# Performance work log

Hardware: AMD Instinct MI355X
Metric: run time of the kernel (lower is better)

The kernel has to match this reference:

```python
import jax, jax.numpy as jnp
import numpy as np

DIM_Q = 1024
DIM_K = 1024
DIM_V = 1024


def setup_inputs() -> dict:
    key = jax.random.key(0)
    kx, kq, kk, kv = jax.random.split(key, 4)
    x = jax.random.normal(kx, (4, 2048, DIM_Q), dtype=jnp.float32)
    # torch nn.Linear weights: [out_features, in_features], y = x @ W.T
    scale = 1.0 / np.sqrt(DIM_Q)
    Wq = jax.random.uniform(kq, (DIM_K, DIM_Q), dtype=jnp.float32, minval=-scale, maxval=scale)
    Wk = jax.random.uniform(kk, (DIM_K, DIM_Q), dtype=jnp.float32, minval=-scale, maxval=scale)
    Wv = jax.random.uniform(kv, (DIM_V, DIM_Q), dtype=jnp.float32, minval=-scale, maxval=scale)
    return {"x": x, "Wq": Wq, "Wk": Wk, "Wv": Wv}


def reference(x, Wq, Wk, Wv):
    # q, k: [b, s, dim_k]; v: [b, s, dim_v]
    q = jnp.einsum('bsd,kd->bsk', x, Wq)
    k = jnp.einsum('bsd,kd->bsk', x, Wk)
    v = jnp.einsum('bsd,vd->bsv', x, Wv)
    norm_fact = 1.0 / jnp.sqrt(jnp.asarray(DIM_K, dtype=x.dtype))
    score = jnp.einsum('bik,bjk->bij', q, k) * norm_fact  # [b, s, s]
    score = jax.nn.softmax(score, axis=-1)
    att = jnp.einsum('bij,bjv->biv', score, v)
    att = att + v  # is_residual=True
    return att
```

## Files before the change

kernel.cpp:

```cpp
#include <hip/hip_runtime.h>
#include <hip/hip_bf16.h>

using bf16 = __hip_bfloat16;
typedef __attribute__((ext_vector_type(8))) short short8;
typedef __attribute__((ext_vector_type(4))) float floatx4;
typedef __attribute__((ext_vector_type(8))) int int8v;

__device__ __forceinline__ void async_ld16(const void* g, void* l) {
  __builtin_amdgcn_global_load_lds((const __attribute__((address_space(1))) void*)g,
                                   (__attribute__((address_space(3))) void*)l, 16, 0, 0);
}

__device__ __forceinline__ int pk4_fp8(float a, float b, float c, float d) {
  int v = __builtin_amdgcn_cvt_pk_fp8_f32(a, b, 0, false);
  return __builtin_amdgcn_cvt_pk_fp8_f32(c, d, v, true);
}

__device__ __forceinline__ int8v ld_frag16(const unsigned char* lo, const unsigned char* hi) {
  int4 l0 = *(const int4*)lo, h0 = *(const int4*)hi;
  int8v v;
  v[0] = l0.x; v[1] = l0.y; v[2] = l0.z; v[3] = l0.w;
  v[4] = h0.x; v[5] = h0.y; v[6] = h0.z; v[7] = h0.w;
  return v;
}


__device__ __forceinline__ void gemm_core(const bf16* __restrict__ At,
                                          const bf16* __restrict__ Bt,
                                          int K, bf16* lA, bf16* lB,
                                          floatx4 acc[4][4]) {
  const int tid  = threadIdx.x;
  const int w    = tid >> 6;
  const int lane = tid & 63;
  const int subM = (w >> 1) * 64;
  const int subN = (w & 1) * 64;
  const int fr   = lane & 15;
  const int fq   = lane >> 4;

  int srow[4], scol[4], sdst[4];
#pragma unroll
  for (int q = 0; q < 4; ++q) {
    int p = q * 256 + w * 64 + lane;
    int r = p >> 3;
    int j = (p & 7) ^ (r & 7);
    srow[q] = r;
    scol[q] = j * 8;
    sdst[q] = (q * 256 + w * 64) * 8;
  }
  int offA[2][4], offB[2][4];
#pragma unroll
  for (int kc = 0; kc < 2; ++kc)
#pragma unroll
    for (int i = 0; i < 4; ++i) {
      int rA = subM + i * 16 + fr;
      offA[kc][i] = (rA * 8 + ((kc * 4 + fq) ^ (rA & 7))) * 8;
      int rB = subN + i * 16 + fr;
      offB[kc][i] = (rB * 8 + ((kc * 4 + fq) ^ (rB & 7))) * 8;
    }

  floatx4 zero = {0.f, 0.f, 0.f, 0.f};
#pragma unroll
  for (int i = 0; i < 4; ++i)
#pragma unroll
    for (int j = 0; j < 4; ++j) acc[i][j] = zero;

  for (int k0 = 0; k0 < K; k0 += 64) {
    __syncthreads();
#pragma unroll
    for (int q = 0; q < 4; ++q) {
      async_ld16(At + (size_t)srow[q] * K + k0 + scol[q], lA + sdst[q]);
      async_ld16(Bt + (size_t)srow[q] * K + k0 + scol[q], lB + sdst[q]);
    }
    __syncthreads();
#pragma unroll
    for (int kc = 0; kc < 2; ++kc) {
      short8 a[4], b[4];
#pragma unroll
      for (int i = 0; i < 4; ++i) a[i] = *(const short8*)(lA + offA[kc][i]);
#pragma unroll
      for (int j = 0; j < 4; ++j) b[j] = *(const short8*)(lB + offB[kc][j]);
#pragma unroll
      for (int i = 0; i < 4; ++i)
#pragma unroll
        for (int j = 0; j < 4; ++j)
          acc[i][j] = __builtin_amdgcn_mfma_f32_16x16x32_bf16(a[i], b[j], acc[i][j], 0, 0, 0);
    }
  }
}

__device__ __forceinline__ void gemm_core_f8(const unsigned char* __restrict__ At,
                                             const unsigned char* __restrict__ Bt,
                                             int K, unsigned char* lA, unsigned char* lB,
                                             floatx4 acc[4][4]) {
  const int tid  = threadIdx.x;
  const int w    = tid >> 6;
  const int lane = tid & 63;
  const int subM = (w >> 1) * 64;
  const int subN = (w & 1) * 64;
  const int fr   = lane & 15;
  const int fq   = lane >> 4;

  int srow[4], scol[4], sdst[4];
#pragma unroll
  for (int q = 0; q < 4; ++q) {
    int p = q * 256 + w * 64 + lane;
    int r = p >> 3;
    int j = (p & 7) ^ (r & 7) ^ ((r & 8) >> 1);
    srow[q] = r;
    scol[q] = j * 16;
    sdst[q] = (q * 256 + w * 64) * 16;
  }
  int offA[2][4], offB[2][4];
#pragma unroll
  for (int h = 0; h < 2; ++h)
#pragma unroll
    for (int i = 0; i < 4; ++i) {
      int rA = subM + i * 16 + fr;
      offA[h][i] = rA * 128 + (((fq * 2 + h) ^ (rA & 7) ^ ((rA & 8) >> 1)) * 16);
      int rB = subN + i * 16 + fr;
      offB[h][i] = rB * 128 + (((fq * 2 + h) ^ (rB & 7) ^ ((rB & 8) >> 1)) * 16);
    }

  floatx4 zero = {0.f, 0.f, 0.f, 0.f};
#pragma unroll
  for (int i = 0; i < 4; ++i)
#pragma unroll
    for (int j = 0; j < 4; ++j) acc[i][j] = zero;

  for (int k0 = 0; k0 < K; k0 += 128) {
    __syncthreads();
#pragma unroll
    for (int q = 0; q < 4; ++q) {
      async_ld16(At + (size_t)srow[q] * K + k0 + scol[q], lA + sdst[q]);
      async_ld16(Bt + (size_t)srow[q] * K + k0 + scol[q], lB + sdst[q]);
    }
    __syncthreads();
    int8v a[4], b[4];
#pragma unroll
    for (int i = 0; i < 4; ++i) a[i] = ld_frag16(lA + offA[0][i], lA + offA[1][i]);
#pragma unroll
    for (int j = 0; j < 4; ++j) b[j] = ld_frag16(lB + offB[0][j], lB + offB[1][j]);
#pragma unroll
    for (int i = 0; i < 4; ++i)
#pragma unroll
      for (int j = 0; j < 4; ++j)
        acc[i][j] = __builtin_amdgcn_mfma_scale_f32_16x16x128_f8f6f4(
            a[i], b[j], acc[i][j], 0, 0, 0, 0x7F7F7F7F, 0, 0x7F7F7F7F);
  }
}

__device__ __forceinline__ void gemm_core_f8_8ph(const unsigned char* __restrict__ At,
                                                 const unsigned char* __restrict__ Bt,
                                                 int K, unsigned char* lds0,
                                                 floatx4 acc[8][4]) {
  const int tid  = threadIdx.x;
  const int w    = tid >> 6;
  const int lane = tid & 63;
  const int wr   = w >> 2;
  const int wc   = w & 3;
  const int subM = wr * 128;
  const int subN = wc * 64;
  const int fr   = lane & 15;
  const int fq   = lane >> 4;

  int srcOff[4], dstOff[4];
#pragma unroll
  for (int q = 0; q < 4; ++q) {
    int p = q * 512 + tid;
    int r = p >> 3;
    int j = (p & 7) ^ (r & 7) ^ ((r & 8) >> 1);
    srcOff[q] = r * K + j * 16;
    dstOff[q] = p * 16;
  }
  int offA[2][8], offB[2][4];
#pragma unroll
  for (int h = 0; h < 2; ++h) {
#pragma unroll
    for (int i = 0; i < 8; ++i) {
      int rA = subM + i * 16 + fr;
      offA[h][i] = rA * 128 + (((fq * 2 + h) ^ (rA & 7) ^ ((rA & 8) >> 1)) * 16);
    }
#pragma unroll
    for (int j = 0; j < 4; ++j) {
      int rB = subN + j * 16 + fr;
      offB[h][j] = rB * 128 + (((fq * 2 + h) ^ (rB & 7) ^ ((rB & 8) >> 1)) * 16);
    }
  }

  auto stageA = [&](int buf, int k0) {
#pragma unroll
    for (int q = 0; q < 4; ++q)
      async_ld16(At + (size_t)(k0 + srcOff[q]), lds0 + buf * 65536 + dstOff[q]);
  };
  auto stageB = [&](int buf, int k0) {
#pragma unroll
    for (int q = 0; q < 4; ++q)
      async_ld16(Bt + (size_t)(k0 + srcOff[q]), lds0 + buf * 65536 + 32768 + dstOff[q]);
  };

  floatx4 zero = {0.f, 0.f, 0.f, 0.f};
#pragma unroll
  for (int i = 0; i < 8; ++i)
#pragma unroll
    for (int j = 0; j < 4; ++j) acc[i][j] = zero;

  stageA(0, 0);
  stageB(0, 0);
  asm volatile("s_waitcnt vmcnt(0)" ::: "memory");
  __builtin_amdgcn_s_barrier();

  const int nt = K >> 7;
  for (int t = 0; t < nt; ++t) {
    const unsigned char* lA = lds0 + (t & 1) * 65536;
    const unsigned char* lB = lA + 32768;
    const int nb = (t + 1) & 1;
    const int k0n = (t + 1) << 7;
    const bool pf = (t + 1) < nt;
    int8v a[4], b0[2], b1[2];

#pragma unroll
    for (int i = 0; i < 4; ++i) a[i] = ld_frag16(lA + offA[0][i], lA + offA[1][i]);
#pragma unroll
    for (int j = 0; j < 2; ++j) b0[j] = ld_frag16(lB + offB[0][j], lB + offB[1][j]);
    if (pf) stageA(nb, k0n);
    __builtin_amdgcn_s_barrier();
    asm volatile("s_waitcnt lgkmcnt(0)" ::: "memory");
    __builtin_amdgcn_sched_barrier(0);
    __builtin_amdgcn_s_setprio(1);
#pragma unroll
    for (int i = 0; i < 4; ++i)
#pragma unroll
      for (int j = 0; j < 2; ++j)
        acc[i][j] = __builtin_amdgcn_mfma_scale_f32_16x16x128_f8f6f4(
            a[i], b0[j], acc[i][j], 0, 0, 0, 0x7F7F7F7F, 0, 0x7F7F7F7F);
    __builtin_amdgcn_s_setprio(0);
    __builtin_amdgcn_s_barrier();

#pragma unroll
    for (int j = 0; j < 2; ++j) b1[j] = ld_frag16(lB + offB[0][2 + j], lB + offB[1][2 + j]);
    if (pf) stageB(nb, k0n);
    __builtin_amdgcn_s_barrier();
    asm volatile("s_waitcnt lgkmcnt(0)" ::: "memory");
    __builtin_amdgcn_sched_barrier(0);
    __builtin_amdgcn_s_setprio(1);
#pragma unroll
    for (int i = 0; i < 4; ++i)
#pragma unroll
      for (int j = 0; j < 2; ++j)
        acc[i][2 + j] = __builtin_amdgcn_mfma_scale_f32_16x16x128_f8f6f4(
            a[i], b1[j], acc[i][2 + j], 0, 0, 0, 0x7F7F7F7F, 0, 0x7F7F7F7F);
    __builtin_amdgcn_s_setprio(0);
    __builtin_amdgcn_s_barrier();

#pragma unroll
    for (int i = 0; i < 4; ++i) a[i] = ld_frag16(lA + offA[0][4 + i], lA + offA[1][4 + i]);
    __builtin_amdgcn_s_barrier();
    asm volatile("s_waitcnt lgkmcnt(0)" ::: "memory");
    __builtin_amdgcn_sched_barrier(0);
    __builtin_amdgcn_s_setprio(1);
#pragma unroll
    for (int i = 0; i < 4; ++i)
#pragma unroll
      for (int j = 0; j < 2; ++j)
        acc[4 + i][2 + j] = __builtin_amdgcn_mfma_scale_f32_16x16x128_f8f6f4(
            a[i], b1[j], acc[4 + i][2 + j], 0, 0, 0, 0x7F7F7F7F, 0, 0x7F7F7F7F);
    __builtin_amdgcn_s_setprio(0);
    __builtin_amdgcn_s_barrier();

#pragma unroll
    for (int j = 0; j < 2; ++j) b0[j] = ld_frag16(lB + offB[0][j], lB + offB[1][j]);
    __builtin_amdgcn_s_barrier();
    asm volatile("s_waitcnt lgkmcnt(0)" ::: "memory");
    __builtin_amdgcn_sched_barrier(0);
    __builtin_amdgcn_s_setprio(1);
#pragma unroll
    for (int i = 0; i < 4; ++i)
#pragma unroll
      for (int j = 0; j < 2; ++j)
        acc[4 + i][j] = __builtin_amdgcn_mfma_scale_f32_16x16x128_f8f6f4(
            a[i], b0[j], acc[4 + i][j], 0, 0, 0, 0x7F7F7F7F, 0, 0x7F7F7F7F);
    __builtin_amdgcn_s_setprio(0);
    asm volatile("s_waitcnt vmcnt(0)" ::: "memory");
    __builtin_amdgcn_s_barrier();
  }
}

__global__ __launch_bounds__(256, 2) void proj_v(
    const bf16* __restrict__ Xbf, const bf16* __restrict__ Wvbf, bf16* __restrict__ Vbf,
    unsigned char* __restrict__ Vt8) {
  __shared__ __align__(16) char lds[49152];
  const int id = blockIdx.x;
  const int tid = threadIdx.x, w = tid >> 6, lane = tid & 63;
  const int fr = lane & 15, fq = lane >> 4;

  const int r = id & 7, g = id >> 3;
  const int ty = r * 8 + (g & 7), tx = g >> 3;
  bf16* lA = (bf16*)lds;
  bf16* lB = (bf16*)(lds + 16384);
  floatx4 acc[4][4];
  gemm_core(Xbf + (size_t)ty * 128 * 1024, Wvbf + (size_t)tx * 128 * 1024,
            1024, lA, lB, acc);
  const int subM = (w >> 1) * 64, subN = (w & 1) * 64;
  const int rowBase = ty * 128 + subM;
  const int colBase = tx * 128 + subN;
#pragma unroll
  for (int i = 0; i < 4; ++i)
#pragma unroll
    for (int j = 0; j < 4; ++j)
#pragma unroll
      for (int rr = 0; rr < 4; ++rr) {
        int row = rowBase + i * 16 + fq * 4 + rr;
        int col = colBase + j * 16 + fr;
        Vbf[(size_t)row * 1024 + col] = __float2bfloat16(acc[i][j][rr]);
      }

  __syncthreads();
  unsigned int* tp = (unsigned int*)lds;
#pragma unroll
  for (int i = 0; i < 4; ++i) {
    int rw = (subM + i * 16 + fq * 4) >> 2;
#pragma unroll
    for (int j = 0; j < 4; ++j) {
      int c = subN + j * 16 + fr;
      tp[c * 32 + (rw ^ (c & 31))] =
          (unsigned int)pk4_fp8(acc[i][j][0], acc[i][j][1], acc[i][j][2], acc[i][j][3]);
    }
  }
  __syncthreads();
  const int vrow = tid >> 1;
  const int gh = tid & 1;
  size_t ob = ((size_t)((ty >> 4) * 1024 + tx * 128 + vrow)) * 2048 +
              (size_t)(ty & 15) * 128 + gh * 64;
#pragma unroll
  for (int h = 0; h < 4; ++h) {
    unsigned int W0 = tp[vrow * 32 + ((gh * 16 + h) ^ (vrow & 31))];
    unsigned int W1 = tp[vrow * 32 + ((gh * 16 + h + 4) ^ (vrow & 31))];
    unsigned int W2 = tp[vrow * 32 + ((gh * 16 + h + 8) ^ (vrow & 31))];
    unsigned int W3 = tp[vrow * 32 + ((gh * 16 + h + 12) ^ (vrow & 31))];
    unsigned int t01l = __builtin_amdgcn_perm(W1, W0, 0x05010400u);
    unsigned int t01h = __builtin_amdgcn_perm(W1, W0, 0x07030602u);
    unsigned int t23l = __builtin_amdgcn_perm(W3, W2, 0x05010400u);
    unsigned int t23h = __builtin_amdgcn_perm(W3, W2, 0x07030602u);
    uint4 o;
    o.x = __builtin_amdgcn_perm(t23l, t01l, 0x05040100u);
    o.y = __builtin_amdgcn_perm(t23l, t01l, 0x07060302u);
    o.z = __builtin_amdgcn_perm(t23h, t01h, 0x05040100u);
    o.w = __builtin_amdgcn_perm(t23h, t01h, 0x07060302u);
    *(uint4*)&Vt8[ob + h * 16] = o;
  }
}

__global__ __launch_bounds__(512, 2) void proj_qk(
    const unsigned char* __restrict__ X8, const unsigned char* __restrict__ Wq8,
    const unsigned char* __restrict__ Wk8,
    unsigned char* __restrict__ Qf8, unsigned char* __restrict__ Kf8) {
  __shared__ __align__(16) char lds[131072];
  const int id = blockIdx.x;
  const int z = id >> 7, lid = id & 127;
  const int ty = lid >> 2, tx = lid & 3;

  floatx4 acc[8][4];
  gemm_core_f8_8ph(X8 + (size_t)ty * 256 * 1024,
                   (z == 0 ? Wq8 : Wk8) + (size_t)tx * 256 * 1024,
                   1024, (unsigned char*)lds, acc);

  unsigned char* dst = (z == 0) ? Qf8 : Kf8;
  const int tid = threadIdx.x, w = tid >> 6, lane = tid & 63;
  const int wr = w >> 2, wc = w & 3;
  const int fr = lane & 15, fq = lane >> 4;
  const int rowBase = ty * 256 + wr * 128;
  const int colBase = tx * 256 + wc * 64;
#pragma unroll
  for (int i = 0; i < 8; ++i)
#pragma unroll
    for (int rr = 0; rr < 4; ++rr) {
      int row = rowBase + i * 16 + fq * 4 + rr;
      unsigned int p0 = (unsigned int)pk4_fp8(acc[i][0][rr], acc[i][1][rr],
                                              acc[i][2][rr], acc[i][3][rr]);
      *(unsigned int*)&dst[(size_t)row * 1024 + colBase + fr * 4] = p0;
    }
}

__global__ __launch_bounds__(512, 2) void mid_kernel(
    const unsigned char* __restrict__ Qf8, const unsigned char* __restrict__ Kf8,
    unsigned char* __restrict__ S8, float* __restrict__ l) {
  __shared__ __align__(16) char lds[131072];
  const int id = blockIdx.x;
  const int b = id >> 6, ty = (id >> 3) & 7, tx = id & 7;

  floatx4 acc[8][4];
  gemm_core_f8_8ph(Qf8 + (size_t)b * 2048 * 1024 + (size_t)ty * 256 * 1024,
                   Kf8 + (size_t)b * 2048 * 1024 + (size_t)tx * 256 * 1024,
                   1024, (unsigned char*)lds, acc);

  const int tid = threadIdx.x, w = tid >> 6, lane = tid & 63;
  const int wr = w >> 2, wc = w & 3;
  const int fr = lane & 15, fq = lane >> 4;
  const int rowBase = ty * 256 + wr * 128;
  const int colBase = tx * 256 + wc * 64;
  unsigned char* Sb = S8 + (size_t)b * 2048 * 2048;
  float* lb = l + (size_t)b * 2048;
#pragma unroll
  for (int i = 0; i < 8; ++i)
#pragma unroll
    for (int rr = 0; rr < 4; ++rr) {
      int row = rowBase + i * 16 + fq * 4 + rr;
      unsigned int p0 = (unsigned int)pk4_fp8(
          __expf(acc[i][0][rr] * 0.03125f), __expf(acc[i][1][rr] * 0.03125f),
          __expf(acc[i][2][rr] * 0.03125f), __expf(acc[i][3][rr] * 0.03125f));
      *(unsigned int*)&Sb[(size_t)row * 2048 + colBase + fr * 4] = p0;
      float psum = __builtin_amdgcn_cvt_f32_fp8(p0, 0) + __builtin_amdgcn_cvt_f32_fp8(p0, 1) +
                   __builtin_amdgcn_cvt_f32_fp8(p0, 2) + __builtin_amdgcn_cvt_f32_fp8(p0, 3);
      psum += __shfl_xor(psum, 1, 64);
      psum += __shfl_xor(psum, 2, 64);
      psum += __shfl_xor(psum, 4, 64);
      psum += __shfl_xor(psum, 8, 64);
      if (fr == 0) atomicAdd(&lb[row], psum);
    }
}

__global__ __launch_bounds__(256, 2) void pv_gemm(const unsigned char* __restrict__ S8,
                                                  const unsigned char* __restrict__ Vt8,
                                                  const bf16* __restrict__ Vbf,
                                                  const float* __restrict__ l,
                                                  float* __restrict__ out) {
  __shared__ __align__(16) char lds[32768];
  unsigned char* lA = (unsigned char*)lds;
  unsigned char* lB = (unsigned char*)(lds + 16384);
  const int id = blockIdx.x;
  const int r = id & 7, g = id >> 3;
  const int b = g >> 4;
  const int rem = g & 15;
  const int ty = r * 2 + (rem & 1);
  const int tx = rem >> 1;

  floatx4 acc[4][4];
  gemm_core_f8(S8 + (size_t)b * 2048 * 2048 + (size_t)ty * 128 * 2048,
               Vt8 + (size_t)b * 1024 * 2048 + (size_t)tx * 128 * 2048,
               2048, lA, lB, acc);

  const int tid = threadIdx.x, w = tid >> 6, lane = tid & 63;
  const int subM = (w >> 1) * 64, subN = (w & 1) * 64;
  const int fr = lane & 15, fq = lane >> 4;
  const int rowBase = ty * 128 + subM;
  const int colBase = tx * 128 + subN;
  const float* lb = l + (size_t)b * 2048;
#pragma unroll
  for (int i = 0; i < 4; ++i)
#pragma unroll
    for (int rr = 0; rr < 4; ++rr) {
      int row = rowBase + i * 16 + fq * 4 + rr;
      float inv = 1.0f / lb[row];
#pragma unroll
      for (int j = 0; j < 4; ++j) {
        int col = colBase + j * 16 + fr;
        size_t oi = ((size_t)b * 2048 + row) * 1024 + col;
        out[oi] = acc[i][j][rr] * inv + __bfloat162float(Vbf[oi]);
      }
    }
}

__global__ void cast_all(const float* __restrict__ x, const float* __restrict__ wq,
                         const float* __restrict__ wk, const float* __restrict__ wv,
                         bf16* __restrict__ Xbf, unsigned char* __restrict__ X8,
                         unsigned char* __restrict__ Wq8, unsigned char* __restrict__ Wk8,
                         bf16* __restrict__ Wvbf, float* __restrict__ l) {
  const int blk = blockIdx.x;
  const int t = threadIdx.x;
  if (blk < 2048) {
#pragma unroll
    for (int k = 0; k < 4; ++k) {
      int i = blk * 1024 + k * 256 + t;
      float4 f = ((const float4*)x)[i];
      bf16 tmp[4] = {__float2bfloat16(f.x), __float2bfloat16(f.y),
                     __float2bfloat16(f.z), __float2bfloat16(f.w)};
      ((ushort4*)Xbf)[i] = *(const ushort4*)tmp;
      ((unsigned int*)X8)[i] = (unsigned int)pk4_fp8(f.x, f.y, f.z, f.w);
    }
  } else if (blk < 2560) {
    const float* src = (blk < 2304) ? wq : wk;
    unsigned char* dst = (blk < 2304) ? Wq8 : Wk8;
    int base = ((blk - 2048) & 255) * 1024;
#pragma unroll
    for (int k = 0; k < 4; ++k) {
      int i = base + k * 256 + t;
      float4 f = ((const float4*)src)[i];
      ((unsigned int*)dst)[i] = (unsigned int)pk4_fp8(f.x, f.y, f.z, f.w);
    }
  } else if (blk < 2816) {
#pragma unroll
    for (int k = 0; k < 4; ++k) {
      int i = (blk - 2560) * 1024 + k * 256 + t;
      float4 f = ((const float4*)wv)[i];
      bf16 tmp[4] = {__float2bfloat16(f.x), __float2bfloat16(f.y),
                     __float2bfloat16(f.z), __float2bfloat16(f.w)};
      ((ushort4*)Wvbf)[i] = *(const ushort4*)tmp;
    }
  } else {
#pragma unroll
    for (int k = 0; k < 8; ++k)
      ((float4*)l)[k * 256 + t] = make_float4(0.f, 0.f, 0.f, 0.f);
  }
}

extern "C" void kernel_launch(void* const* d_in, const int* in_sizes, int n_in,
                              void* d_out, int out_size, void* d_ws, size_t ws_size,
                              hipStream_t stream) {
  const float* x  = (const float*)d_in[0];
  const float* Wq = (const float*)d_in[1];
  const float* Wk = (const float*)d_in[2];
  const float* Wv = (const float*)d_in[3];
  float* out = (float*)d_out;

  char* ws = (char*)d_ws;
  bf16* Xbf = (bf16*)ws;                   ws += (size_t)8192 * 1024 * 2;
  unsigned char* X8 = (unsigned char*)ws;  ws += (size_t)8192 * 1024;
  unsigned char* Wq8 = (unsigned char*)ws; ws += (size_t)1024 * 1024;
  unsigned char* Wk8 = (unsigned char*)ws; ws += (size_t)1024 * 1024;
  bf16* Wvbf = (bf16*)ws;                  ws += (size_t)1024 * 1024 * 2;
  unsigned char* Qf8 = (unsigned char*)ws; ws += (size_t)8192 * 1024;
  unsigned char* Kf8 = (unsigned char*)ws; ws += (size_t)8192 * 1024;
  bf16* Vbf = (bf16*)ws;                   ws += (size_t)8192 * 1024 * 2;
  unsigned char* Vt8 = (unsigned char*)ws; ws += (size_t)4 * 1024 * 2048;
  unsigned char* S8  = (unsigned char*)ws; ws += (size_t)4 * 2048 * 2048;
  float* l = (float*)ws;                   ws += (size_t)8192 * 4;

  cast_all<<<2817, 256, 0, stream>>>(x, Wq, Wk, Wv, Xbf, X8, Wq8, Wk8, Wvbf, l);
  proj_v<<<512, 256, 0, stream>>>(Xbf, Wvbf, Vbf, Vt8);
  proj_qk<<<256, 512, 0, stream>>>(X8, Wq8, Wk8, Qf8, Kf8);
  mid_kernel<<<256, 512, 0, stream>>>(Qf8, Kf8, S8, l);
  pv_gemm<<<512, 256, 0, stream>>>(S8, Vt8, Vbf, l, out);
}
```

Measured before the change: 188.1 us.

## Split fp8 GEMM tile loads into four sub-stages with partial vmcnt waits

Reorganizes the async global-to-LDS loading in the fp8 8-phase GEMM core into four row-interleaved sub-stages (A and B halves), issued at two points per iteration. Loads are always issued, wrapping to tile zero on the last iteration so the vmcnt count stays constant. Waits use vmcnt(4) instead of draining all loads, so part of the next tile can stay in flight across barriers. This aims to hide global-load latency behind MFMA work, at the cost of redundant loads on the final iteration and a more fragile correctness argument about which rows are ready before they are read.

```diff
diff --git a/kernel.cpp b/kernel.cpp
--- a/kernel.cpp
+++ b/kernel.cpp
@@ -163,15 +163,23 @@
   const int fr   = lane & 15;
   const int fq   = lane >> 4;
 
-  int srcOff[4], dstOff[4];
-#pragma unroll
-  for (int q = 0; q < 4; ++q) {
-    int p = q * 512 + tid;
-    int r = p >> 3;
-    int j = (p & 7) ^ (r & 7) ^ ((r & 8) >> 1);
-    srcOff[q] = r * K + j * 16;
-    dstOff[q] = p * 16;
-  }
+  int srcOff[4][2], dstOff[4][2];
+#pragma unroll
+  for (int s = 0; s < 4; ++s)
+#pragma unroll
+    for (int ldi = 0; ldi < 2; ++ldi) {
+      int c = ldi * 512 + tid;
+      int rs = c >> 3;
+      int row;
+      if (s == 0)      row = (rs < 64) ? rs : rs + 64;
+      else if (s == 2) row = 64 + ((rs < 64) ? rs : rs + 64);
+      else if (s == 1) row = (rs & 31) + (rs >> 5) * 64;
+      else             row = 32 + (rs & 31) + (rs >> 5) * 64;
+      int j = (c & 7) ^ (row & 7) ^ ((row & 8) >> 1);
+      srcOff[s][ldi] = row * K + j * 16;
+      dstOff[s][ldi] = row * 128 + (c & 7) * 16;
+    }
+
   int offA[2][8], offB[2][4];
 #pragma unroll
   for (int h = 0; h < 2; ++h) {
@@ -187,16 +195,12 @@
     }
   }
 
-  auto stageA = [&](int buf, int k0) {
-#pragma unroll
-    for (int q = 0; q < 4; ++q)
-      async_ld16(At + (size_t)(k0 + srcOff[q]), lds0 + buf * 65536 + dstOff[q]);
+  auto stage = [&](int buf, int k0, int s) {
+    const unsigned char* src = (s & 1) ? Bt : At;
+    unsigned char* dstb = lds0 + buf * 65536 + ((s & 1) ? 32768 : 0);
+    async_ld16(src + (size_t)(k0 + srcOff[s][0]), dstb + dstOff[s][0]);
+    async_ld16(src + (size_t)(k0 + srcOff[s][1]), dstb + dstOff[s][1]);
   };
-  auto stageB = [&](int buf, int k0) {
-#pragma unroll
-    for (int q = 0; q < 4; ++q)
-      async_ld16(Bt + (size_t)(k0 + srcOff[q]), lds0 + buf * 65536 + 32768 + dstOff[q]);
-  };
 
   floatx4 zero = {0.f, 0.f, 0.f, 0.f};
 #pragma unroll
@@ -204,25 +208,28 @@
 #pragma unroll
     for (int j = 0; j < 4; ++j) acc[i][j] = zero;
 
-  stageA(0, 0);
-  stageB(0, 0);
-  asm volatile("s_waitcnt vmcnt(0)" ::: "memory");
+  const int nt = K >> 7;
+  stage(0, 0, 0);
+  stage(0, 0, 1);
+  stage(0, 0, 2);
+  stage(0, 0, 3);
+  asm volatile("s_waitcnt vmcnt(4)" ::: "memory");
   __builtin_amdgcn_s_barrier();
 
-  const int nt = K >> 7;
   for (int t = 0; t < nt; ++t) {
     const unsigned char* lA = lds0 + (t & 1) * 65536;
     const unsigned char* lB = lA + 32768;
     const int nb = (t + 1) & 1;
-    const int k0n = (t + 1) << 7;
-    const bool pf = (t + 1) < nt;
+    const int tn = (t + 1 < nt) ? (t + 1) : 0;
+    const int k0n = tn << 7;
     int8v a[4], b0[2], b1[2];
 
 #pragma unroll
     for (int i = 0; i < 4; ++i) a[i] = ld_frag16(lA + offA[0][i], lA + offA[1][i]);
 #pragma unroll
     for (int j = 0; j < 2; ++j) b0[j] = ld_frag16(lB + offB[0][j], lB + offB[1][j]);
-    if (pf) stageA(nb, k0n);
+    stage(nb, k0n, 0);
+    stage(nb, k0n, 1);
     __builtin_amdgcn_s_barrier();
     asm volatile("s_waitcnt lgkmcnt(0)" ::: "memory");
     __builtin_amdgcn_sched_barrier(0);
@@ -234,11 +241,13 @@
         acc[i][j] = __builtin_amdgcn_mfma_scale_f32_16x16x128_f8f6f4(
             a[i], b0[j], acc[i][j], 0, 0, 0, 0x7F7F7F7F, 0, 0x7F7F7F7F);
     __builtin_amdgcn_s_setprio(0);
+    asm volatile("s_waitcnt vmcnt(4)" ::: "memory");
     __builtin_amdgcn_s_barrier();
 
 #pragma unroll
     for (int j = 0; j < 2; ++j) b1[j] = ld_frag16(lB + offB[0][2 + j], lB + offB[1][2 + j]);
-    if (pf) stageB(nb, k0n);
+    stage(nb, k0n, 2);
+    stage(nb, k0n, 3);
     __builtin_amdgcn_s_barrier();
     asm volatile("s_waitcnt lgkmcnt(0)" ::: "memory");
     __builtin_amdgcn_sched_barrier(0);
@@ -280,9 +289,10 @@
         acc[4 + i][j] = __builtin_amdgcn_mfma_scale_f32_16x16x128_f8f6f4(
             a[i], b0[j], acc[4 + i][j], 0, 0, 0, 0x7F7F7F7F, 0, 0x7F7F7F7F);
     __builtin_amdgcn_s_setprio(0);
-    asm volatile("s_waitcnt vmcnt(0)" ::: "memory");
-    __builtin_amdgcn_s_barrier();
-  }
+    asm volatile("s_waitcnt vmcnt(4)" ::: "memory");
+    __builtin_amdgcn_s_barrier();
+  }
+  asm volatile("s_waitcnt vmcnt(0)" ::: "memory");
 }
 
 __global__ __launch_bounds__(256, 2) void proj_v(
```

Measured after the change: 187.2 us. Within noise of the previous version (-0.5%).
